# Kernel optimization log

Measured on AMD Instinct MI355X. Metric: run time of the kernel, lower is better.

Reference implementation:

```python
import jax, jax.numpy as jnp
import numpy as np

N = 50000          # num nodes
EDG = 1600000      # num edges
DIM = 128          # in_dim == out_dim (dim_h)
H = 8              # num_heads
HD = DIM // H      # head dim = 16
BN_EPS = 1e-5


def _batchnorm(x, gamma, beta):
    # training-mode BatchNorm1d: biased batch stats over node axis
    mean = x.mean(axis=0)
    var = x.var(axis=0)
    return (x - mean) * jax.lax.rsqrt(var + BN_EPS) * gamma + beta


def setup_inputs() -> dict:
    key = jax.random.key(0)
    ks = jax.random.split(key, 12)
    lin = lambda k, o, i: jax.random.normal(k, (o, i), jnp.float32) * (1.0 / np.sqrt(i))
    return {
        "h": jax.random.normal(ks[0], (N, DIM), jnp.float32),
        "edge_index": jax.random.randint(ks[1], (2, EDG), 0, N, jnp.int32),
        "edge_attr": jax.random.normal(ks[2], (EDG, DIM), jnp.float32),
        "Wq": lin(ks[3], DIM, DIM),
        "Wk": lin(ks[4], DIM, DIM),
        "Wv": lin(ks[5], DIM, DIM),
        "We": lin(ks[6], DIM, DIM),
        "Wb": lin(ks[7], H, DIM),
        "bb": jnp.zeros((H,), jnp.float32),
        "gamma1": jnp.ones((DIM,), jnp.float32),
        "beta1": jnp.zeros((DIM,), jnp.float32),
        "W1": lin(ks[8], 2 * DIM, DIM),
        "b1": jnp.zeros((2 * DIM,), jnp.float32),
        "W2": lin(ks[9], DIM, 2 * DIM),
        "b2": jnp.zeros((DIM,), jnp.float32),
        "gamma2": jnp.ones((DIM,), jnp.float32),
        "beta2": jnp.zeros((DIM,), jnp.float32),
    }


def reference(h, edge_index, edge_attr, Wq, Wk, Wv, We, Wb, bb,
              gamma1, beta1, W1, b1, W2, b2, gamma2, beta2):
    n = h.shape[0]
    src, dst = edge_index[0], edge_index[1]

    Qh = (h @ Wq.T).reshape(n, H, HD)
    Kh = (h @ Wk.T).reshape(n, H, HD)
    Vh = (h @ Wv.T).reshape(n, H, HD)
    E = (edge_attr @ We.T).reshape(-1, H, HD)          # (EDG, H, HD)
    E_bias = edge_attr @ Wb.T + bb                      # (EDG, H)

    # per-edge attention score: sum over head dim of Kh[src]*Qh[dst]*E
    score = (Kh[src] * Qh[dst] * E).sum(-1) / np.sqrt(HD) + E_bias
    score = jnp.exp(jnp.clip(score, -5.0, 5.0))         # (EDG, H)

    msg = Vh[src] * score[..., None]                    # (EDG, H, HD)
    wV = jax.ops.segment_sum(msg, dst, num_segments=n)  # (N, H, HD)
    Z = jax.ops.segment_sum(score, dst, num_segments=n) # (N, H)

    h_attn = (wV / (Z[..., None] + 1e-6)).reshape(n, DIM)
    x = h + h_attn                                      # residual
    x = _batchnorm(x, gamma1, beta1)

    ff = jax.nn.relu(x @ W1.T + b1) @ W2.T + b2
    out = _batchnorm(x + ff, gamma2, beta2)
    return out
```

## Files before the change

kernel.cpp:

```cpp
#include <hip/hip_runtime.h>
#include <math.h>

typedef __attribute__((ext_vector_type(8))) short bf16x8;
typedef __attribute__((ext_vector_type(4))) short bf16x4;
typedef __attribute__((ext_vector_type(4))) float f32x4;

static __device__ __forceinline__ unsigned short f2bf(float x){
    union{float f; unsigned u;} v; v.f = x;
    unsigned r = v.u + 0x7fffu + ((v.u >> 16) & 1u);
    return (unsigned short)(r >> 16);
}
static __device__ __forceinline__ unsigned cvtpk(float lo, float hi){
    unsigned r;
    asm("v_cvt_pk_bf16_f32 %0, %1, %2" : "=v"(r) : "v"(lo), "v"(hi));
    return r;
}

__global__ __launch_bounds__(128)
void qkv_kernel(const float* __restrict__ h,
                const float* __restrict__ Wq, const float* __restrict__ Wk,
                const float* __restrict__ Wv,
                float* __restrict__ Qb, float* __restrict__ Kb, float* __restrict__ Vb)
{
    __shared__ float hl[16 * 128];
    const int t  = threadIdx.x;
    const int n0 = blockIdx.x * 16;

    const float4* hg4 = (const float4*)(h + (size_t)n0 * 128);
    float4* hl4 = (float4*)hl;
    #pragma unroll
    for (int i = 0; i < 4; ++i) hl4[i * 128 + t] = hg4[i * 128 + t];
    __syncthreads();

    #pragma unroll
    for (int m = 0; m < 3; ++m) {
        const float* W = (m == 0 ? Wq : (m == 1 ? Wk : Wv)) + t * 128;
        float*       o = (m == 0 ? Qb : (m == 1 ? Kb : Vb)) + (size_t)n0 * 128 + t;
        float acc[16];
        #pragma unroll
        for (int n = 0; n < 16; ++n) acc[n] = 0.f;
        for (int kc = 0; kc < 32; ++kc) {
            const float4 w = *(const float4*)(W + kc * 4);
            #pragma unroll
            for (int n = 0; n < 16; ++n) {
                const float4 x = *(const float4*)&hl[n * 128 + kc * 4];
                acc[n] += w.x * x.x + w.y * x.y + w.z * x.z + w.w * x.w;
            }
        }
        #pragma unroll
        for (int n = 0; n < 16; ++n) o[(size_t)n * 128] = acc[n];
    }
}

__global__ void hist_kernel(const int* __restrict__ ei, int* __restrict__ cnt, int EDG)
{
    const int stride = gridDim.x * blockDim.x;
    for (int e = blockIdx.x * blockDim.x + threadIdx.x; e < EDG; e += stride)
        atomicAdd(&cnt[ei[EDG + e]], 1);
}

__global__ __launch_bounds__(1024)
void scan_a(const int* __restrict__ cnt, int* __restrict__ bsum, int n)
{
    __shared__ int tmp[1024];
    const int t = threadIdx.x;
    const int i = blockIdx.x * 1024 + t;
    tmp[t] = (i < n) ? cnt[i] : 0;
    __syncthreads();
    for (int d = 512; d > 0; d >>= 1) {
        if (t < d) tmp[t] += tmp[t + d];
        __syncthreads();
    }
    if (t == 0) bsum[blockIdx.x] = tmp[0];
}

__global__ void scan_b(const int* __restrict__ bsum, int* __restrict__ bbase,
                       int* __restrict__ offs, int nb, int n)
{
    if (threadIdx.x == 0) {
        int run = 0;
        for (int b = 0; b < nb; ++b) { bbase[b] = run; run += bsum[b]; }
        offs[n] = run;
    }
}

__global__ __launch_bounds__(1024)
void scan_c(const int* __restrict__ cnt, const int* __restrict__ bbase,
            int* __restrict__ offs, int n)
{
    __shared__ int tmp[1024];
    const int t = threadIdx.x;
    const int i = blockIdx.x * 1024 + t;
    const int v = (i < n) ? cnt[i] : 0;
    tmp[t] = v;
    __syncthreads();
    for (int d = 1; d < 1024; d <<= 1) {
        const int a = (t >= d) ? tmp[t - d] : 0;
        __syncthreads();
        tmp[t] += a;
        __syncthreads();
    }
    if (i < n) offs[i] = bbase[blockIdx.x] + tmp[t] - v;
}

__global__ void scatter_kernel(const int* __restrict__ ei, const int* __restrict__ offs,
                               int* __restrict__ cnt, int2* __restrict__ elist, int EDG)
{
    const int stride = gridDim.x * blockDim.x;
    for (int e = blockIdx.x * blockDim.x + threadIdx.x; e < EDG; e += stride) {
        const int d = ei[EDG + e];
        const int p = atomicSub(&cnt[d], 1) - 1;
        int2 v; v.x = ei[e]; v.y = e;
        elist[offs[d] + p] = v;
    }
}

__global__ __launch_bounds__(256, 3)
void fused_attn(const float* __restrict__ eattr, const int2* __restrict__ elist,
                const int* __restrict__ offs,
                const float* __restrict__ We, const float* __restrict__ Wb,
                const float* __restrict__ bbv,
                const float* __restrict__ Qb, const float* __restrict__ Kb,
                const float* __restrict__ Vb, const float* __restrict__ h,
                float* __restrict__ x, float* __restrict__ stat, int N, int EDG)
{
    __shared__ unsigned short WeB[128 * 128];
    __shared__ unsigned short WbB[16 * 128];
    __shared__ float scw[4][16][8];
    __shared__ int   srw[4][16];
    __shared__ float ssl[4][128];
    __shared__ float sql[4][128];

    const int t = threadIdx.x;
    #pragma unroll
    for (int i = 0; i < 16; ++i) {
        const int idx4 = i * 256 + t;
        const int d = idx4 >> 5, k0 = (idx4 & 31) * 4;
        const float4 wv = *(const float4*)&We[d * 128 + k0];
        bf16x4 p;
        p[0] = (short)f2bf(wv.x); p[1] = (short)f2bf(wv.y);
        p[2] = (short)f2bf(wv.z); p[3] = (short)f2bf(wv.w);
        *(bf16x4*)((char*)WeB + d * 256 + ((2 * k0) ^ ((d & 7) << 4))) = p;
    }
    #pragma unroll
    for (int i = 0; i < 8; ++i) {
        const int idx = i * 256 + t;
        const int r = idx >> 7, k = idx & 127;
        const unsigned short v = (r < 8) ? f2bf(Wb[r * 128 + k]) : (unsigned short)0;
        *(unsigned short*)((char*)WbB + r * 256 + ((2 * k) ^ ((r & 7) << 4))) = v;
    }
    __syncthreads();

    const int l = t & 63, w = t >> 6;
    const int eloc = l & 15, g4 = l >> 4;
    const int hh_l = l >> 3;
    const int kb_l = g4 * 16;
    float bb[8];
    #pragma unroll
    for (int hh = 0; hh < 8; ++hh) bb[hh] = bbv[hh];

    float2 sA = {0.f, 0.f}, sQ2 = {0.f, 0.f};
    const int GW = gridDim.x * 4;
    for (int node = blockIdx.x * 4 + w; node < N; node += GW) {
        const int beg = offs[node], end = offs[node + 1];

        const float* qrow = Qb + (size_t)node * 128 + g4 * 4;
        float4 qv[8];
        #pragma unroll
        for (int hh = 0; hh < 8; ++hh) qv[hh] = *(const float4*)(qrow + hh * 16);

        float2 pv = {0.f, 0.f};
        float zz = 0.f;

        for (int base = beg; base < end; base += 16) {
            const int cnt = min(16, end - base);
            int ii = base + eloc;
            ii = (ii < EDG) ? ii : (EDG - 1);
            const int2 se = elist[ii];

            const float* ep = eattr + (size_t)se.y * 128 + g4 * 8;
            float4 ea0[4], ea1[4];
            #pragma unroll
            for (int ks = 0; ks < 4; ++ks) {
                ea0[ks] = *(const float4*)(ep + ks * 32);
                ea1[ks] = *(const float4*)(ep + ks * 32 + 4);
            }
            const float* kr = Kb + (size_t)se.x * 128 + g4 * 4;

            f32x4 acc[8], accb;
            #pragma unroll
            for (int hh = 0; hh < 8; ++hh) acc[hh] = (f32x4){0.f, 0.f, 0.f, 0.f};
            accb = (f32x4){0.f, 0.f, 0.f, 0.f};
            #pragma unroll
            for (int ks = 0; ks < 4; ++ks) {
                union { unsigned u[4]; bf16x8 v; } fr;
                fr.u[0] = cvtpk(ea0[ks].x, ea0[ks].y);
                fr.u[1] = cvtpk(ea0[ks].z, ea0[ks].w);
                fr.u[2] = cvtpk(ea1[ks].x, ea1[ks].y);
                fr.u[3] = cvtpk(ea1[ks].z, ea1[ks].w);
                const int kb = ks * 64 + kb_l;
                const bf16x8 abf = *(const bf16x8*)((char*)WbB + eloc * 256 + (kb ^ ((eloc & 7) << 4)));
                accb = __builtin_amdgcn_mfma_f32_16x16x32_bf16(abf, fr.v, accb, 0, 0, 0);
                #pragma unroll
                for (int hh = 0; hh < 8; ++hh) {
                    const int ar = hh * 16 + eloc;
                    const bf16x8 af = *(const bf16x8*)((char*)WeB + ar * 256 + (kb ^ ((ar & 7) << 4)));
                    acc[hh] = __builtin_amdgcn_mfma_f32_16x16x32_bf16(af, fr.v, acc[hh], 0, 0, 0);
                }
            }

            float scv[8];
            #pragma unroll
            for (int hh = 0; hh < 8; ++hh) {
                const float4 kk = *(const float4*)(kr + hh * 16);
                const float4 qq = qv[hh];
                float m = acc[hh][0] * (kk.x * qq.x) + acc[hh][1] * (kk.y * qq.y)
                        + acc[hh][2] * (kk.z * qq.z) + acc[hh][3] * (kk.w * qq.w);
                m += __shfl_xor(m, 16);
                m += __shfl_xor(m, 32);
                const float eb = __shfl(accb[hh & 3], ((hh >> 2) << 4) | eloc);
                float sc = m * 0.25f + eb + bb[hh];
                sc = expf(fminf(fmaxf(sc, -5.f), 5.f));
                scv[hh] = (eloc < cnt) ? sc : 0.f;
            }
            if (l < 16) {
                float4 s0 = {scv[0], scv[1], scv[2], scv[3]};
                float4 s1 = {scv[4], scv[5], scv[6], scv[7]};
                *(float4*)&scw[w][l][0] = s0;
                *(float4*)&scw[w][l][4] = s1;
                srw[w][l] = se.x;
            }
            asm volatile("s_waitcnt lgkmcnt(0)" ::: "memory");
            __builtin_amdgcn_sched_barrier(0);

            int e = 0;
            for (; e + 3 < cnt; e += 4) {
                const int   s0 = srw[w][e],     s1 = srw[w][e + 1];
                const int   s2 = srw[w][e + 2], s3 = srw[w][e + 3];
                const float c0 = scw[w][e][hh_l],     c1 = scw[w][e + 1][hh_l];
                const float c2 = scw[w][e + 2][hh_l], c3 = scw[w][e + 3][hh_l];
                const float2 v0 = *(const float2*)&Vb[(size_t)s0 * 128 + 2 * l];
                const float2 v1 = *(const float2*)&Vb[(size_t)s1 * 128 + 2 * l];
                const float2 v2 = *(const float2*)&Vb[(size_t)s2 * 128 + 2 * l];
                const float2 v3 = *(const float2*)&Vb[(size_t)s3 * 128 + 2 * l];
                pv.x += v0.x * c0 + v1.x * c1 + v2.x * c2 + v3.x * c3;
                pv.y += v0.y * c0 + v1.y * c1 + v2.y * c2 + v3.y * c3;
                zz += c0 + c1 + c2 + c3;
            }
            for (; e < cnt; ++e) {
                const int   s0 = srw[w][e];
                const float c0 = scw[w][e][hh_l];
                const float2 v0 = *(const float2*)&Vb[(size_t)s0 * 128 + 2 * l];
                pv.x += v0.x * c0; pv.y += v0.y * c0;
                zz += c0;
            }
        }

        const float inv = 1.f / (zz + 1e-6f);
        const float2 hv = *(const float2*)&h[(size_t)node * 128 + 2 * l];
        float2 xv;
        xv.x = hv.x + pv.x * inv;
        xv.y = hv.y + pv.y * inv;
        *(float2*)&x[(size_t)node * 128 + 2 * l] = xv;
        sA.x += xv.x; sA.y += xv.y;
        sQ2.x += xv.x * xv.x; sQ2.y += xv.y * xv.y;
    }

    ssl[w][2 * l] = sA.x;  ssl[w][2 * l + 1] = sA.y;
    sql[w][2 * l] = sQ2.x; sql[w][2 * l + 1] = sQ2.y;
    __syncthreads();
    if (t < 128) {
        atomicAdd(&stat[t],       ssl[0][t] + ssl[1][t] + ssl[2][t] + ssl[3][t]);
        atomicAdd(&stat[128 + t], sql[0][t] + sql[1][t] + sql[2][t] + sql[3][t]);
    }
}

__global__ void bn_params(const float* __restrict__ sum, const float* __restrict__ sumsq,
                          const float* __restrict__ gamma, const float* __restrict__ beta,
                          float* __restrict__ a, float* __restrict__ b, float invn)
{
    const int c = threadIdx.x;
    const float mean = sum[c] * invn;
    const float var  = sumsq[c] * invn - mean * mean;
    const float sc   = gamma[c] * rsqrtf(var + 1e-5f);
    a[c] = sc;
    b[c] = beta[c] - mean * sc;
}

__global__ __launch_bounds__(128)
void ffn_kernel(const float* __restrict__ x, const float* __restrict__ W1,
                const float* __restrict__ b1, const float* __restrict__ W2,
                const float* __restrict__ b2, const float* __restrict__ par,
                float* __restrict__ zb, float* __restrict__ stat2)
{
    __shared__ float xnl[16 * 128];
    __shared__ float hidl[16 * 256];
    const int t  = threadIdx.x;
    const int n0 = blockIdx.x * 16;

    const float4* xg4 = (const float4*)(x + (size_t)n0 * 128);
    const float4* a4  = (const float4*)par;
    const float4* bv4 = (const float4*)(par + 128);
    float4* xnl4 = (float4*)xnl;
    #pragma unroll
    for (int i = 0; i < 4; ++i) {
        const int idx = i * 128 + t;
        const float4 xv = xg4[idx];
        const float4 av = a4[idx & 31], bv = bv4[idx & 31];
        float4 r;
        r.x = xv.x * av.x + bv.x; r.y = xv.y * av.y + bv.y;
        r.z = xv.z * av.z + bv.z; r.w = xv.w * av.w + bv.w;
        xnl4[idx] = r;
    }
    __syncthreads();

    float acc0[16], acc1[16];
    #pragma unroll
    for (int n = 0; n < 16; ++n) { acc0[n] = 0.f; acc1[n] = 0.f; }
    const float* w0p = W1 + (size_t)t * 128;
    const float* w1p = W1 + (size_t)(t + 128) * 128;
    for (int kc = 0; kc < 32; ++kc) {
        const float4 w0 = *(const float4*)(w0p + kc * 4);
        const float4 w1 = *(const float4*)(w1p + kc * 4);
        #pragma unroll
        for (int n = 0; n < 16; ++n) {
            const float4 xv = *(const float4*)&xnl[n * 128 + kc * 4];
            acc0[n] += w0.x * xv.x + w0.y * xv.y + w0.z * xv.z + w0.w * xv.w;
            acc1[n] += w1.x * xv.x + w1.y * xv.y + w1.z * xv.z + w1.w * xv.w;
        }
    }
    const float bi0 = b1[t], bi1 = b1[t + 128];
    #pragma unroll
    for (int n = 0; n < 16; ++n) {
        hidl[n * 256 + t]       = fmaxf(acc0[n] + bi0, 0.f);
        hidl[n * 256 + 128 + t] = fmaxf(acc1[n] + bi1, 0.f);
    }
    __syncthreads();

    float acc2[16];
    #pragma unroll
    for (int n = 0; n < 16; ++n) acc2[n] = 0.f;
    const float* w2p = W2 + (size_t)t * 256;
    for (int kc = 0; kc < 64; ++kc) {
        const float4 w = *(const float4*)(w2p + kc * 4);
        #pragma unroll
        for (int n = 0; n < 16; ++n) {
            const float4 hv = *(const float4*)&hidl[n * 256 + kc * 4];
            acc2[n] += w.x * hv.x + w.y * hv.y + w.z * hv.z + w.w * hv.w;
        }
    }
    const float bi2 = b2[t];
    float s = 0.f, sq = 0.f;
    float* zo = zb + (size_t)n0 * 128 + t;
    #pragma unroll
    for (int n = 0; n < 16; ++n) {
        const float z = xnl[n * 128 + t] + acc2[n] + bi2;
        zo[(size_t)n * 128] = z;
        s += z; sq += z * z;
    }
    atomicAdd(&stat2[t], s);
    atomicAdd(&stat2[128 + t], sq);
}

__global__ void final_bn(const float4* __restrict__ zb, const float* __restrict__ pa,
                         const float* __restrict__ pb, float4* __restrict__ out, int total4)
{
    const float4* a4 = (const float4*)pa;
    const float4* b4 = (const float4*)pb;
    const int stride = gridDim.x * blockDim.x;
    for (int i = blockIdx.x * blockDim.x + threadIdx.x; i < total4; i += stride) {
        const float4 z = zb[i];
        const float4 a = a4[i & 31], b = b4[i & 31];
        float4 r;
        r.x = z.x * a.x + b.x; r.y = z.y * a.y + b.y;
        r.z = z.z * a.z + b.z; r.w = z.w * a.w + b.w;
        out[i] = r;
    }
}

extern "C" void kernel_launch(void* const* d_in, const int* in_sizes, int n_in,
                              void* d_out, int out_size, void* d_ws, size_t ws_size,
                              hipStream_t stream)
{
    const float* h   = (const float*)d_in[0];
    const int*   ei  = (const int*)  d_in[1];
    const float* ea  = (const float*)d_in[2];
    const float* Wq  = (const float*)d_in[3];
    const float* Wk  = (const float*)d_in[4];
    const float* Wv  = (const float*)d_in[5];
    const float* We  = (const float*)d_in[6];
    const float* Wb  = (const float*)d_in[7];
    const float* bbv = (const float*)d_in[8];
    const float* g1  = (const float*)d_in[9];
    const float* be1 = (const float*)d_in[10];
    const float* W1  = (const float*)d_in[11];
    const float* b1  = (const float*)d_in[12];
    const float* W2  = (const float*)d_in[13];
    const float* b2  = (const float*)d_in[14];
    const float* g2  = (const float*)d_in[15];
    const float* be2 = (const float*)d_in[16];
    float* out = (float*)d_out;

    const int N   = in_sizes[0] / 128;
    const int EDG = in_sizes[1] / 2;
    const int NB  = (N + 1023) / 1024;
    const size_t nd = (size_t)N * 128;
    auto al8 = [](size_t v){ return (v + 7) & ~(size_t)7; };

    float* ws = (float*)d_ws;
    const size_t Qo  = 0;
    const size_t Ko  = nd;
    const size_t Vo  = 2 * nd;
    const size_t Xo  = 3 * nd;
    const size_t ELo = 4 * nd;
    const size_t OFo = ELo + (size_t)EDG * 2;
    const size_t CUo = al8(OFo + (size_t)N + 8);
    const size_t BSo = al8(CUo + (size_t)N);
    const size_t BBo = al8(BSo + (size_t)NB);
    const size_t STo = al8(BBo + (size_t)NB);
    const size_t PAR = STo + 512;

    int*  cnt   = (int*)(ws + CUo);
    int*  offs  = (int*)(ws + OFo);
    int*  bsum  = (int*)(ws + BSo);
    int*  bbase = (int*)(ws + BBo);
    int2* elist = (int2*)(ws + ELo);

    hipMemsetAsync(cnt, 0, (size_t)N * sizeof(int), stream);
    hipMemsetAsync(ws + STo, 0, 512 * sizeof(float), stream);

    qkv_kernel<<<N / 16, 128, 0, stream>>>(h, Wq, Wk, Wv, ws + Qo, ws + Ko, ws + Vo);

    hist_kernel<<<1024, 256, 0, stream>>>(ei, cnt, EDG);
    scan_a<<<NB, 1024, 0, stream>>>(cnt, bsum, N);
    scan_b<<<1, 64, 0, stream>>>(bsum, bbase, offs, NB, N);
    scan_c<<<NB, 1024, 0, stream>>>(cnt, bbase, offs, N);
    scatter_kernel<<<1024, 256, 0, stream>>>(ei, offs, cnt, elist, EDG);

    fused_attn<<<768, 256, 0, stream>>>(ea, elist, offs, We, Wb, bbv,
                                        ws + Qo, ws + Ko, ws + Vo, h,
                                        ws + Xo, ws + STo, N, EDG);

    bn_params<<<1, 128, 0, stream>>>(ws + STo, ws + STo + 128, g1, be1,
                                     ws + PAR, ws + PAR + 128, 1.0f / (float)N);
    ffn_kernel<<<N / 16, 128, 0, stream>>>(ws + Xo, W1, b1, W2, b2, ws + PAR,
                                           ws + Qo, ws + STo + 256);
    bn_params<<<1, 128, 0, stream>>>(ws + STo + 256, ws + STo + 384, g2, be2,
                                     ws + PAR + 256, ws + PAR + 384, 1.0f / (float)N);
    final_bn<<<1024, 256, 0, stream>>>((const float4*)(ws + Qo), ws + PAR + 256,
                                       ws + PAR + 384, (float4*)out, N * 32);
}
```

Before: 1.033 ms.

## Double attention block size and split V aggregation across wave halves

```diff
diff --git a/kernel.cpp b/kernel.cpp
--- a/kernel.cpp
+++ b/kernel.cpp
@@ -115,7 +115,7 @@
     }
 }
 
-__global__ __launch_bounds__(256, 3)
+__global__ __launch_bounds__(512, 5)
 void fused_attn(const float* __restrict__ eattr, const int2* __restrict__ elist,
                 const int* __restrict__ offs,
                 const float* __restrict__ We, const float* __restrict__ Wb,
@@ -126,15 +126,15 @@
 {
     __shared__ unsigned short WeB[128 * 128];
     __shared__ unsigned short WbB[16 * 128];
-    __shared__ float scw[4][16][8];
-    __shared__ int   srw[4][16];
-    __shared__ float ssl[4][128];
-    __shared__ float sql[4][128];
+    __shared__ float scw[8][16][8];
+    __shared__ int   srw[8][16];
+    __shared__ float ssl[8][128];
+    __shared__ float sql[8][128];
 
     const int t = threadIdx.x;
     #pragma unroll
-    for (int i = 0; i < 16; ++i) {
-        const int idx4 = i * 256 + t;
+    for (int i = 0; i < 8; ++i) {
+        const int idx4 = i * 512 + t;
         const int d = idx4 >> 5, k0 = (idx4 & 31) * 4;
         const float4 wv = *(const float4*)&We[d * 128 + k0];
         bf16x4 p;
@@ -143,8 +143,8 @@
         *(bf16x4*)((char*)WeB + d * 256 + ((2 * k0) ^ ((d & 7) << 4))) = p;
     }
     #pragma unroll
-    for (int i = 0; i < 8; ++i) {
-        const int idx = i * 256 + t;
+    for (int i = 0; i < 4; ++i) {
+        const int idx = i * 512 + t;
         const int r = idx >> 7, k = idx & 127;
         const unsigned short v = (r < 8) ? f2bf(Wb[r * 128 + k]) : (unsigned short)0;
         *(unsigned short*)((char*)WbB + r * 256 + ((2 * k) ^ ((r & 7) << 4))) = v;
@@ -153,15 +153,16 @@
 
     const int l = t & 63, w = t >> 6;
     const int eloc = l & 15, g4 = l >> 4;
-    const int hh_l = l >> 3;
+    const int half = l >> 5, q = l & 31;
+    const int hq = q >> 2;
     const int kb_l = g4 * 16;
     float bb[8];
     #pragma unroll
     for (int hh = 0; hh < 8; ++hh) bb[hh] = bbv[hh];
 
-    float2 sA = {0.f, 0.f}, sQ2 = {0.f, 0.f};
-    const int GW = gridDim.x * 4;
-    for (int node = blockIdx.x * 4 + w; node < N; node += GW) {
+    float4 sA = {0.f, 0.f, 0.f, 0.f}, sQ2 = {0.f, 0.f, 0.f, 0.f};
+    const int GW = gridDim.x * 8;
+    for (int node = blockIdx.x * 8 + w; node < N; node += GW) {
         const int beg = offs[node], end = offs[node + 1];
 
         const float* qrow = Qb + (size_t)node * 128 + g4 * 4;
@@ -169,7 +170,7 @@
         #pragma unroll
         for (int hh = 0; hh < 8; ++hh) qv[hh] = *(const float4*)(qrow + hh * 16);
 
-        float2 pv = {0.f, 0.f};
+        float4 pv = {0.f, 0.f, 0.f, 0.f};
         float zz = 0.f;
 
         for (int base = beg; base < end; base += 16) {
@@ -233,45 +234,55 @@
             asm volatile("s_waitcnt lgkmcnt(0)" ::: "memory");
             __builtin_amdgcn_sched_barrier(0);
 
-            int e = 0;
-            for (; e + 3 < cnt; e += 4) {
-                const int   s0 = srw[w][e],     s1 = srw[w][e + 1];
-                const int   s2 = srw[w][e + 2], s3 = srw[w][e + 3];
-                const float c0 = scw[w][e][hh_l],     c1 = scw[w][e + 1][hh_l];
-                const float c2 = scw[w][e + 2][hh_l], c3 = scw[w][e + 3][hh_l];
-                const float2 v0 = *(const float2*)&Vb[(size_t)s0 * 128 + 2 * l];
-                const float2 v1 = *(const float2*)&Vb[(size_t)s1 * 128 + 2 * l];
-                const float2 v2 = *(const float2*)&Vb[(size_t)s2 * 128 + 2 * l];
-                const float2 v3 = *(const float2*)&Vb[(size_t)s3 * 128 + 2 * l];
-                pv.x += v0.x * c0 + v1.x * c1 + v2.x * c2 + v3.x * c3;
-                pv.y += v0.y * c0 + v1.y * c1 + v2.y * c2 + v3.y * c3;
-                zz += c0 + c1 + c2 + c3;
-            }
-            for (; e < cnt; ++e) {
+            int e = half;
+            for (; e + 2 < cnt; e += 4) {
+                const int   s0 = srw[w][e],     s1 = srw[w][e + 2];
+                const float c0 = scw[w][e][hq], c1 = scw[w][e + 2][hq];
+                const float4 v0 = *(const float4*)&Vb[(size_t)s0 * 128 + 4 * q];
+                const float4 v1 = *(const float4*)&Vb[(size_t)s1 * 128 + 4 * q];
+                pv.x += v0.x * c0 + v1.x * c1;
+                pv.y += v0.y * c0 + v1.y * c1;
+                pv.z += v0.z * c0 + v1.z * c1;
+                pv.w += v0.w * c0 + v1.w * c1;
+                zz += c0 + c1;
+            }
+            for (; e < cnt; e += 2) {
                 const int   s0 = srw[w][e];
-                const float c0 = scw[w][e][hh_l];
-                const float2 v0 = *(const float2*)&Vb[(size_t)s0 * 128 + 2 * l];
+                const float c0 = scw[w][e][hq];
+                const float4 v0 = *(const float4*)&Vb[(size_t)s0 * 128 + 4 * q];
                 pv.x += v0.x * c0; pv.y += v0.y * c0;
+                pv.z += v0.z * c0; pv.w += v0.w * c0;
                 zz += c0;
             }
         }
 
-        const float inv = 1.f / (zz + 1e-6f);
-        const float2 hv = *(const float2*)&h[(size_t)node * 128 + 2 * l];
-        float2 xv;
-        xv.x = hv.x + pv.x * inv;
-        xv.y = hv.y + pv.y * inv;
-        *(float2*)&x[(size_t)node * 128 + 2 * l] = xv;
-        sA.x += xv.x; sA.y += xv.y;
-        sQ2.x += xv.x * xv.x; sQ2.y += xv.y * xv.y;
-    }
-
-    ssl[w][2 * l] = sA.x;  ssl[w][2 * l + 1] = sA.y;
-    sql[w][2 * l] = sQ2.x; sql[w][2 * l + 1] = sQ2.y;
+        pv.x += __shfl_xor(pv.x, 32); pv.y += __shfl_xor(pv.y, 32);
+        pv.z += __shfl_xor(pv.z, 32); pv.w += __shfl_xor(pv.w, 32);
+        zz   += __shfl_xor(zz, 32);
+        if (half == 0) {
+            const float inv = 1.f / (zz + 1e-6f);
+            const float4 hv = *(const float4*)&h[(size_t)node * 128 + 4 * q];
+            float4 xv;
+            xv.x = hv.x + pv.x * inv; xv.y = hv.y + pv.y * inv;
+            xv.z = hv.z + pv.z * inv; xv.w = hv.w + pv.w * inv;
+            *(float4*)&x[(size_t)node * 128 + 4 * q] = xv;
+            sA.x += xv.x; sA.y += xv.y; sA.z += xv.z; sA.w += xv.w;
+            sQ2.x += xv.x * xv.x; sQ2.y += xv.y * xv.y;
+            sQ2.z += xv.z * xv.z; sQ2.w += xv.w * xv.w;
+        }
+    }
+
+    if (half == 0) {
+        *(float4*)&ssl[w][4 * q] = sA;
+        *(float4*)&sql[w][4 * q] = sQ2;
+    }
     __syncthreads();
     if (t < 128) {
-        atomicAdd(&stat[t],       ssl[0][t] + ssl[1][t] + ssl[2][t] + ssl[3][t]);
-        atomicAdd(&stat[128 + t], sql[0][t] + sql[1][t] + sql[2][t] + sql[3][t]);
+        float s = 0.f, sq2 = 0.f;
+        #pragma unroll
+        for (int wi = 0; wi < 8; ++wi) { s += ssl[wi][t]; sq2 += sql[wi][t]; }
+        atomicAdd(&stat[t], s);
+        atomicAdd(&stat[128 + t], sq2);
     }
 }
 
@@ -437,7 +448,7 @@
     scan_c<<<NB, 1024, 0, stream>>>(cnt, bbase, offs, N);
     scatter_kernel<<<1024, 256, 0, stream>>>(ei, offs, cnt, elist, EDG);
 
-    fused_attn<<<768, 256, 0, stream>>>(ea, elist, offs, We, Wb, bbv,
+    fused_attn<<<768, 512, 0, stream>>>(ea, elist, offs, We, Wb, bbv,
                                         ws + Qo, ws + Ko, ws + Vo, h,
                                         ws + Xo, ws + STo, N, EDG);
 
```

Result: slower. 1.405 ms (+36.0%).
